# Kernel optimization log

Hardware: AMD Instinct MI355X
Metric: run time of the kernel (lower is better)

## Reference

```python
import jax, jax.numpy as jnp
import numpy as np

S = 4096      # seq_len
D = 1024      # d_model
H = 16        # n_heads
E = 64        # head dim (D // H)
SCALE0 = 1.0 / np.sqrt(E)  # sh_scale_factor


def setup_inputs() -> dict:
    key = jax.random.key(0)
    ks = jax.random.split(key, 10)
    std = 1.0 / np.sqrt(D)
    inputs = jax.random.normal(ks[0], (S, D), dtype=jnp.float32)
    # per-head projection weights stacked over heads: [H, D, E]
    Wq = jax.random.normal(ks[1], (H, D, E), dtype=jnp.float32) * std
    bq = jnp.zeros((H, E), dtype=jnp.float32)
    Wk = jax.random.normal(ks[2], (H, D, E), dtype=jnp.float32) * std
    bk = jnp.zeros((H, E), dtype=jnp.float32)
    Wv = jax.random.normal(ks[3], (H, D, E), dtype=jnp.float32) * std
    bv = jnp.zeros((H, E), dtype=jnp.float32)
    # learned per-head scalar scale, initialized to 1/sqrt(E)
    scale = jnp.full((H,), SCALE0, dtype=jnp.float32)
    # output projection (stored as [D_in, D_out])
    Wo = jax.random.normal(ks[4], (H * E, D), dtype=jnp.float32) * std
    bo = jnp.zeros((D,), dtype=jnp.float32)
    return {"inputs": inputs, "Wq": Wq, "bq": bq, "Wk": Wk, "bk": bk,
            "Wv": Wv, "bv": bv, "scale": scale, "Wo": Wo, "bo": bo}


def reference(inputs, Wq, bq, Wk, bk, Wv, bv, scale, Wo, bo):
    # per-head QKV projections, batched over heads: [H, S, E]
    q = jnp.einsum('sd,hde->hse', inputs, Wq) + bq[:, None, :]
    k = jnp.einsum('sd,hde->hse', inputs, Wk) + bk[:, None, :]
    v = jnp.einsum('sd,hde->hse', inputs, Wv) + bv[:, None, :]
    # scores [H, S, S], learned scalar scale per head, softmax over keys
    scores = jnp.einsum('hqe,hke->hqk', q, k) * scale[:, None, None]
    attn = jax.nn.softmax(scores, axis=-1)
    o = jnp.einsum('hqk,hke->hqe', attn, v)           # [H, S, E]
    o = jnp.transpose(o, (1, 0, 2)).reshape(S, H * E)  # concat heads on dim 1
    return o @ Wo + bo                                 # [S, D]
```

## Files before the change

kernel.cpp:

```cpp
#include <hip/hip_runtime.h>
#include <stdint.h>

#define S_LEN 4096
#define D_MOD 1024
#define NH    16
#define EH    64

typedef short bf16x8 __attribute__((ext_vector_type(8)));
typedef float f32x4  __attribute__((ext_vector_type(4)));
typedef float f32x16 __attribute__((ext_vector_type(16)));

__device__ __forceinline__ unsigned short f2b(float x){
    uint32_t u = __float_as_uint(x);
    u = (u + 0x7fffu + ((u >> 16) & 1u)) >> 16;
    return (unsigned short)u;
}

__device__ __forceinline__ uint32_t cvtpk_bf16(float lo, float hi){
    uint32_t r;
    asm volatile("v_cvt_pk_bf16_f32 %0, %1, %2" : "=v"(r) : "v"(lo), "v"(hi));
    return r;
}

__device__ __forceinline__ void gld_lds16(const void* g, void* l){
    __builtin_amdgcn_global_load_lds((const __attribute__((address_space(1))) void*)g,
                                     (__attribute__((address_space(3))) void*)l, 16, 0, 0);
}

#define PSWAP_U(a, b) asm volatile("v_permlane32_swap_b32 %0, %1" : "+v"(a), "+v"(b))

#define WAITV4() asm volatile("s_waitcnt vmcnt(4)" ::: "memory")
#define WAITV0() asm volatile("s_waitcnt vmcnt(0)" ::: "memory")
#define CFENCE() asm volatile("" ::: "memory")


__global__ void k_conv_all(const float* __restrict__ x, unsigned short* __restrict__ xb,
                           const float* __restrict__ Wq, const float* __restrict__ Wk,
                           const float* __restrict__ Wv, unsigned short* __restrict__ wt,
                           const float* __restrict__ Wo, unsigned short* __restrict__ wot){
    __shared__ float lt[64][65];
    const int tid = threadIdx.x;
    int b = blockIdx.x;
    if (b < 4096){
        int i = (b * 256 + tid) * 4;
        float4 v = *(const float4*)(x + i);
        ushort4 o;
        o.x = f2b(v.x); o.y = f2b(v.y); o.z = f2b(v.z); o.w = f2b(v.w);
        *(ushort4*)(xb + i) = o;
        return;
    }
    b -= 4096;
    if (b < 768){
        const int d0 = (b & 15) * 64;
        const int th = b >> 4;
        const int t = th >> 4, h = th & 15;
        const float* W = (t == 0) ? Wq : ((t == 1) ? Wk : Wv);
        #pragma unroll
        for (int i = 0; i < 16; i++){
            int idx = tid + 256 * i;
            int dl = idx >> 6, e = idx & 63;
            lt[dl][e] = W[((size_t)((h << 10) + d0 + dl) << 6) + e];
        }
        __syncthreads();
        #pragma unroll
        for (int i = 0; i < 16; i++){
            int idx = tid + 256 * i;
            int eo = idx >> 6, dlo = idx & 63;
            wt[((size_t)((t << 10) + (h << 6) + eo) << 10) + d0 + dlo] = f2b(lt[dlo][eo]);
        }
    } else {
        b -= 768;
        const int he0 = (b & 15) * 64, d0 = (b >> 4) * 64;
        #pragma unroll
        for (int i = 0; i < 16; i++){
            int idx = tid + 256 * i;
            int r = idx >> 6, c = idx & 63;
            lt[r][c] = Wo[((size_t)(he0 + r) << 10) + d0 + c];
        }
        __syncthreads();
        #pragma unroll
        for (int i = 0; i < 16; i++){
            int idx = tid + 256 * i;
            int rr = idx >> 6, cc = idx & 63;
            wot[((size_t)(d0 + rr) << 10) + he0 + cc] = f2b(lt[cc][rr]);
        }
    }
}

__global__ void k_tv(const unsigned short* __restrict__ vr, unsigned short* __restrict__ vt){
    __shared__ unsigned short lt[64][66];
    const int tid = threadIdx.x;
    const int s0 = blockIdx.x * 64, h = blockIdx.y;
    #pragma unroll
    for (int i = 0; i < 4; i++){
        int idx = tid + 256 * i;
        int r = idx >> 4, c4 = idx & 15;
        ushort4 v = *(const ushort4*)(vr + (((size_t)(h << 12) + s0 + r) << 6) + c4 * 4);
        lt[r][c4 * 4 + 0] = v.x; lt[r][c4 * 4 + 1] = v.y;
        lt[r][c4 * 4 + 2] = v.z; lt[r][c4 * 4 + 3] = v.w;
    }
    __syncthreads();
    #pragma unroll
    for (int i = 0; i < 4; i++){
        int idx = tid + 256 * i;
        int e = idx >> 4, j4 = idx & 15;
        ushort4 o;
        o.x = lt[j4 * 4 + 0][e]; o.y = lt[j4 * 4 + 1][e];
        o.z = lt[j4 * 4 + 2][e]; o.w = lt[j4 * 4 + 3][e];
        *(ushort4*)(vt + (size_t)((h << 6) + e) * 4096 + s0 + j4 * 4) = o;
    }
}


template<int MODE, int NI>
__global__ __launch_bounds__(256, 4)
void k_gemm(const unsigned short* __restrict__ A, const unsigned short* __restrict__ B, int K,
            unsigned short* __restrict__ qb, unsigned short* __restrict__ kb,
            unsigned short* __restrict__ vr,
            const float* __restrict__ b0, const float* __restrict__ b1, const float* __restrict__ b2,
            const float* __restrict__ scl,
            float* __restrict__ outp, const float* __restrict__ bo){
    __shared__ uint4 lsA4[1024];
    __shared__ uint4 lsB4[NI * 256];
    char* lsA = (char*)lsA4;
    char* lsB = (char*)lsB4;
    const int tid = threadIdx.x;
    const int lane = tid & 63, w = tid >> 6;
    const int lr = lane & 15, lg = lane >> 4;
    const int wm = w >> 1, wn = w & 1;
    const int m0 = blockIdx.y * 128, n0 = blockIdx.x * (32 * NI);
    const int wbase = tid & ~63;

    f32x4 acc[4][NI] = {};

    for (int k0 = 0; k0 < K; k0 += 64){
        __syncthreads();
        #pragma unroll
        for (int i = 0; i < 4; i++){
            int s = tid + 256 * i;
            int row = s >> 3, c = s & 7;
            int cs = c ^ (row & 7);
            gld_lds16(A + (size_t)(m0 + row) * K + k0 + cs * 8, lsA + (wbase + 256 * i) * 16);
        }
        #pragma unroll
        for (int i = 0; i < NI; i++){
            int s = tid + 256 * i;
            int row = s >> 3, c = s & 7;
            int cs = c ^ (row & 7);
            gld_lds16(B + (size_t)(n0 + row) * K + k0 + cs * 8, lsB + (wbase + 256 * i) * 16);
        }
        __syncthreads();
        #pragma unroll
        for (int kc = 0; kc < 2; kc++){
            bf16x8 af[4], bf[NI];
            #pragma unroll
            for (int mi = 0; mi < 4; mi++){
                int row = wm * 64 + mi * 16 + lr;
                int j = kc * 4 + lg;
                af[mi] = *(const bf16x8*)(lsA + row * 128 + (j ^ (row & 7)) * 16);
            }
            #pragma unroll
            for (int ni = 0; ni < NI; ni++){
                int row = wn * (NI * 16) + ni * 16 + lr;
                int j = kc * 4 + lg;
                bf[ni] = *(const bf16x8*)(lsB + row * 128 + (j ^ (row & 7)) * 16);
            }
            #pragma unroll
            for (int mi = 0; mi < 4; mi++)
                #pragma unroll
                for (int ni = 0; ni < NI; ni++)
                    acc[mi][ni] = __builtin_amdgcn_mfma_f32_16x16x32_bf16(af[mi], bf[ni], acc[mi][ni], 0, 0, 0);
        }
    }

    #pragma unroll
    for (int mi = 0; mi < 4; mi++){
        #pragma unroll
        for (int ni = 0; ni < NI; ni++){
            int gnb = n0 + wn * (NI * 16) + ni * 16;
            if (MODE == 0){
                int t = gnb >> 10, h = (gnb >> 6) & 15;
                int e = (gnb & 63) + lr;
                const float* bp = (t == 0) ? b0 : ((t == 1) ? b1 : b2);
                float badd = bp[(h << 6) + e];
                float qs = (t == 0) ? scl[h] * 1.4426950408889634f : 1.0f;
                unsigned short* tgt = (t == 0) ? qb : ((t == 1) ? kb : vr);
                #pragma unroll
                for (int r = 0; r < 4; r++){
                    int gm = m0 + wm * 64 + mi * 16 + lg * 4 + r;
                    tgt[((size_t)((h << 12) + gm) << 6) + e] = f2b((acc[mi][ni][r] + badd) * qs);
                }
            } else {
                int gn = gnb + lr;
                float badd = bo[gn];
                #pragma unroll
                for (int r = 0; r < 4; r++){
                    int gm = m0 + wm * 64 + mi * 16 + lg * 4 + r;
                    outp[(size_t)gm * 1024 + gn] = acc[mi][ni][r] + badd;
                }
            }
        }
    }
}


__global__ __launch_bounds__(256, 4)
void k_attn(const unsigned short* __restrict__ qb, const unsigned short* __restrict__ kb,
            const unsigned short* __restrict__ vt,
            unsigned short* __restrict__ po0, unsigned short* __restrict__ po1,
            float* __restrict__ pl){
    __shared__ uint4 ldsb[2048];
    char* ldsc = (char*)ldsb;

    const int tid = threadIdx.x;
    const int lane = tid & 63, w = tid >> 6;
    const int ql = lane & 31, hi = lane >> 5;

    int wg = blockIdx.y * 64 + blockIdx.x;
    wg = (wg & 7) * 128 + (wg >> 3);
    const int h = wg >> 6;
    const int qblk = (wg & 63) >> 1;
    const int sk = wg & 1;
    const int q0 = qblk * 128 + w * 32;
    const int kbase = sk * 2048;

    bf16x8 qf[4];
    #pragma unroll
    for (int kc = 0; kc < 4; kc++)
        qf[kc] = *(const bf16x8*)(qb + (size_t)((h << 12) + q0 + ql) * 64 + kc * 16 + hi * 8);

    bf16x8 ones;
    #pragma unroll
    for (int j = 0; j < 8; j++) ones[j] = (short)0x3F80;

    f32x16 oacc[2] = {}, lacc = {};

    auto stage = [&](int buf, int kt){
        char* Kd = ldsc + buf * 16384;
        char* Vd = Kd + 8192;
        #pragma unroll
        for (int c = 0; c < 2; c++){
            int g = w * 2 + c;
            const unsigned short* ksrc = kb + ((size_t)(h << 12) + kt + (g >> 2) * 32 + ql) * 64
                                            + (g & 3) * 16 + hi * 8;
            gld_lds16(ksrc, Kd + g * 1024);
            const unsigned short* vsrc = vt + (size_t)((h << 6) + (g >> 2) * 32 + ql) * 4096
                                            + kt + (g & 3) * 16 + hi * 8;
            gld_lds16(vsrc, Vd + g * 1024);
        }
    };

    auto pack2 = [&](f32x16& v, bf16x8& pA, bf16x8& pB){
        #pragma unroll
        for (int r = 0; r < 16; r++)
            v[r] = __builtin_amdgcn_exp2f(v[r]);
        uint32_t a0 = cvtpk_bf16(v[0], v[1]);
        uint32_t a1 = cvtpk_bf16(v[2], v[3]);
        uint32_t b0 = cvtpk_bf16(v[4], v[5]);
        uint32_t b1 = cvtpk_bf16(v[6], v[7]);
        PSWAP_U(a0, b0);
        PSWAP_U(a1, b1);
        uint32_t f0[4] = {a0, a1, b0, b1};
        pA = *(bf16x8*)f0;
        uint32_t c0 = cvtpk_bf16(v[8],  v[9]);
        uint32_t c1 = cvtpk_bf16(v[10], v[11]);
        uint32_t d0 = cvtpk_bf16(v[12], v[13]);
        uint32_t d1 = cvtpk_bf16(v[14], v[15]);
        PSWAP_U(c0, d0);
        PSWAP_U(c1, d1);
        uint32_t f1[4] = {c0, c1, d0, d1};
        pB = *(bf16x8*)f1;
    };

    stage(0, kbase);
    stage(1, kbase + 64);

    int buf = 0;
    for (int t = 0; t < 32; t++){
        if (t < 31) WAITV4();
        else        WAITV0();
        __builtin_amdgcn_s_barrier();
        CFENCE();

        const char* Kc = ldsc + buf * 16384;
        const char* Vc = Kc + 8192;

        f32x16 s0 = {}, s1 = {};
        __builtin_amdgcn_s_setprio(1);
        #pragma unroll
        for (int kc = 0; kc < 4; kc++){
            bf16x8 kf = *(const bf16x8*)(Kc + kc * 1024 + lane * 16);
            s0 = __builtin_amdgcn_mfma_f32_32x32x16_bf16(kf, qf[kc], s0, 0, 0, 0);
        }
        #pragma unroll
        for (int kc = 0; kc < 4; kc++){
            bf16x8 kf = *(const bf16x8*)(Kc + (4 + kc) * 1024 + lane * 16);
            s1 = __builtin_amdgcn_mfma_f32_32x32x16_bf16(kf, qf[kc], s1, 0, 0, 0);
        }
        bf16x8 p00, p01;
        pack2(s0, p00, p01);

        {
            bf16x8 vf0 = *(const bf16x8*)(Vc + (0 * 4 + 0) * 1024 + lane * 16);
            oacc[0] = __builtin_amdgcn_mfma_f32_32x32x16_bf16(vf0, p00, oacc[0], 0, 0, 0);
            bf16x8 vf1 = *(const bf16x8*)(Vc + (1 * 4 + 0) * 1024 + lane * 16);
            oacc[1] = __builtin_amdgcn_mfma_f32_32x32x16_bf16(vf1, p00, oacc[1], 0, 0, 0);
            lacc = __builtin_amdgcn_mfma_f32_32x32x16_bf16(ones, p00, lacc, 0, 0, 0);
            bf16x8 vf2 = *(const bf16x8*)(Vc + (0 * 4 + 1) * 1024 + lane * 16);
            oacc[0] = __builtin_amdgcn_mfma_f32_32x32x16_bf16(vf2, p01, oacc[0], 0, 0, 0);
            bf16x8 vf3 = *(const bf16x8*)(Vc + (1 * 4 + 1) * 1024 + lane * 16);
            oacc[1] = __builtin_amdgcn_mfma_f32_32x32x16_bf16(vf3, p01, oacc[1], 0, 0, 0);
            lacc = __builtin_amdgcn_mfma_f32_32x32x16_bf16(ones, p01, lacc, 0, 0, 0);
        }
        bf16x8 p10, p11;
        pack2(s1, p10, p11);

        {
            bf16x8 vf0 = *(const bf16x8*)(Vc + (0 * 4 + 2) * 1024 + lane * 16);
            oacc[0] = __builtin_amdgcn_mfma_f32_32x32x16_bf16(vf0, p10, oacc[0], 0, 0, 0);
            bf16x8 vf1 = *(const bf16x8*)(Vc + (1 * 4 + 2) * 1024 + lane * 16);
            oacc[1] = __builtin_amdgcn_mfma_f32_32x32x16_bf16(vf1, p10, oacc[1], 0, 0, 0);
            lacc = __builtin_amdgcn_mfma_f32_32x32x16_bf16(ones, p10, lacc, 0, 0, 0);
            bf16x8 vf2 = *(const bf16x8*)(Vc + (0 * 4 + 3) * 1024 + lane * 16);
            oacc[0] = __builtin_amdgcn_mfma_f32_32x32x16_bf16(vf2, p11, oacc[0], 0, 0, 0);
            bf16x8 vf3 = *(const bf16x8*)(Vc + (1 * 4 + 3) * 1024 + lane * 16);
            oacc[1] = __builtin_amdgcn_mfma_f32_32x32x16_bf16(vf3, p11, oacc[1], 0, 0, 0);
            lacc = __builtin_amdgcn_mfma_f32_32x32x16_bf16(ones, p11, lacc, 0, 0, 0);
        }
        __builtin_amdgcn_s_setprio(0);
        CFENCE();

        if (t + 2 < 32){
            __builtin_amdgcn_s_barrier();
            CFENCE();
            stage(buf, kbase + (t + 2) * 64);
        }
        buf ^= 1;
    }

    unsigned short* pout = sk ? po1 : po0;
    if (lane < 32)
        pl[((sk << 4) + h) * 4096 + q0 + ql] = lacc[0];
    #pragma unroll
    for (int et = 0; et < 2; et++){
        #pragma unroll
        for (int g = 0; g < 4; g++){
            ushort4 o4;
            o4.x = f2b(oacc[et][4 * g + 0]);
            o4.y = f2b(oacc[et][4 * g + 1]);
            o4.z = f2b(oacc[et][4 * g + 2]);
            o4.w = f2b(oacc[et][4 * g + 3]);
            int e = et * 32 + 8 * g + 4 * hi;
            *(ushort4*)(pout + (size_t)(q0 + ql) * 1024 + (h << 6) + e) = o4;
        }
    }
}

__global__ void k_comb(const unsigned short* __restrict__ po0, const unsigned short* __restrict__ po1,
                       const float* __restrict__ pl, unsigned short* __restrict__ ob){
    int i = blockIdx.x * 256 + threadIdx.x;
    int s = i >> 7, g8 = i & 127;
    int h = g8 >> 3;
    float inv = 1.0f / (pl[(h << 12) + s] + pl[((16 + h) << 12) + s]);
    size_t off = ((size_t)s << 10) + g8 * 8;
    const ushort4* a = (const ushort4*)(po0 + off);
    const ushort4* b = (const ushort4*)(po1 + off);
    ushort4 o[2];
    #pragma unroll
    for (int k = 0; k < 2; k++){
        ushort4 av = a[k], bv = b[k];
        o[k].x = f2b((__uint_as_float((uint32_t)av.x << 16) + __uint_as_float((uint32_t)bv.x << 16)) * inv);
        o[k].y = f2b((__uint_as_float((uint32_t)av.y << 16) + __uint_as_float((uint32_t)bv.y << 16)) * inv);
        o[k].z = f2b((__uint_as_float((uint32_t)av.z << 16) + __uint_as_float((uint32_t)bv.z << 16)) * inv);
        o[k].w = f2b((__uint_as_float((uint32_t)av.w << 16) + __uint_as_float((uint32_t)bv.w << 16)) * inv);
    }
    *(ushort4*)(ob + off) = o[0];
    *(ushort4*)(ob + off + 4) = o[1];
}


extern "C" void kernel_launch(void* const* d_in, const int* in_sizes, int n_in,
                              void* d_out, int out_size, void* d_ws, size_t ws_size,
                              hipStream_t stream){
    const float* x  = (const float*)d_in[0];
    const float* Wq = (const float*)d_in[1];
    const float* bq = (const float*)d_in[2];
    const float* Wk = (const float*)d_in[3];
    const float* bk = (const float*)d_in[4];
    const float* Wv = (const float*)d_in[5];
    const float* bv = (const float*)d_in[6];
    const float* sc = (const float*)d_in[7];
    const float* Wo = (const float*)d_in[8];
    const float* bo = (const float*)d_in[9];
    float* out = (float*)d_out;
    char* ws = (char*)d_ws;
    const size_t MB = 1u << 20;

    unsigned short* xb  = (unsigned short*)(ws + 0);
    unsigned short* ob  = xb;
    unsigned short* wt  = (unsigned short*)(ws + 8  * MB);
    unsigned short* wot = (unsigned short*)(ws + 14 * MB);
    unsigned short* qb  = (unsigned short*)(ws + 16 * MB);
    unsigned short* kb  = (unsigned short*)(ws + 24 * MB);
    unsigned short* vr  = (unsigned short*)(ws + 32 * MB);
    unsigned short* po0 = vr;
    unsigned short* vt  = (unsigned short*)(ws + 40 * MB);
    unsigned short* po1 = (unsigned short*)(ws + 48 * MB);
    float*          pl  = (float*)(ws + 56 * MB);

    k_conv_all<<<5120, 256, 0, stream>>>(x, xb, Wq, Wk, Wv, wt, Wo, wot);

    k_gemm<0, 4><<<dim3(24, 32), 256, 0, stream>>>(xb, wt, D_MOD, qb, kb, vr, bq, bk, bv, sc, nullptr, nullptr);
    k_tv        <<<dim3(64, 16), 256, 0, stream>>>(vr, vt);
    k_attn      <<<dim3(64, 16), 256, 0, stream>>>(qb, kb, vt, po0, po1, pl);
    k_comb      <<<2048, 256, 0, stream>>>(po0, po1, pl, ob);
    k_gemm<1, 2><<<dim3(16, 32), 256, 0, stream>>>(ob, wot, D_MOD, nullptr, nullptr, nullptr,
                                                   nullptr, nullptr, nullptr, nullptr, out, bo);
}
```

Before: 160.0 us.

## Process two query tiles per wave and replace ones-MFMA row sums with VALU sums

```diff
diff --git a/kernel.cpp b/kernel.cpp
--- a/kernel.cpp
+++ b/kernel.cpp
@@ -28,6 +28,17 @@
 }
 
 #define PSWAP_U(a, b) asm volatile("v_permlane32_swap_b32 %0, %1" : "+v"(a), "+v"(b))
+
+__device__ __forceinline__ float vcopy(float x){
+    float y;
+    asm volatile("v_mov_b32 %0, %1" : "=v"(y) : "v"(x));
+    return y;
+}
+__device__ __forceinline__ float pswap_add(float x){
+    uint32_t a = __float_as_uint(x), b = __float_as_uint(vcopy(x));
+    PSWAP_U(a, b);
+    return __uint_as_float(a) + __uint_as_float(b);
+}
 
 #define WAITV4() asm volatile("s_waitcnt vmcnt(4)" ::: "memory")
 #define WAITV0() asm volatile("s_waitcnt vmcnt(0)" ::: "memory")
@@ -204,7 +215,7 @@
 }
 
 
-__global__ __launch_bounds__(256, 4)
+__global__ __launch_bounds__(256, 2)
 void k_attn(const unsigned short* __restrict__ qb, const unsigned short* __restrict__ kb,
             const unsigned short* __restrict__ vt,
             unsigned short* __restrict__ po0, unsigned short* __restrict__ po1,
@@ -216,24 +227,23 @@
     const int lane = tid & 63, w = tid >> 6;
     const int ql = lane & 31, hi = lane >> 5;
 
-    int wg = blockIdx.y * 64 + blockIdx.x;
-    wg = (wg & 7) * 128 + (wg >> 3);
-    const int h = wg >> 6;
-    const int qblk = (wg & 63) >> 1;
-    const int sk = wg & 1;
-    const int q0 = qblk * 128 + w * 32;
+    int wg = blockIdx.y * 32 + blockIdx.x;
+    wg = (wg & 7) * 64 + (wg >> 3);
+    const int h = wg >> 5;
+    const int rem = wg & 31;
+    const int qblk = rem >> 1, sk = rem & 1;
+    const int q0 = qblk * 256 + w * 64;
     const int kbase = sk * 2048;
 
-    bf16x8 qf[4];
-    #pragma unroll
-    for (int kc = 0; kc < 4; kc++)
-        qf[kc] = *(const bf16x8*)(qb + (size_t)((h << 12) + q0 + ql) * 64 + kc * 16 + hi * 8);
-
-    bf16x8 ones;
-    #pragma unroll
-    for (int j = 0; j < 8; j++) ones[j] = (short)0x3F80;
-
-    f32x16 oacc[2] = {}, lacc = {};
+    bf16x8 qf0[4], qf1[4];
+    #pragma unroll
+    for (int kc = 0; kc < 4; kc++){
+        qf0[kc] = *(const bf16x8*)(qb + (size_t)((h << 12) + q0 + ql) * 64 + kc * 16 + hi * 8);
+        qf1[kc] = *(const bf16x8*)(qb + (size_t)((h << 12) + q0 + 32 + ql) * 64 + kc * 16 + hi * 8);
+    }
+
+    f32x16 o00 = {}, o01 = {}, o10 = {}, o11 = {};
+    float ps0 = 0.f, ps1 = 0.f;
 
     auto stage = [&](int buf, int kt){
         char* Kd = ldsc + buf * 16384;
@@ -250,10 +260,12 @@
         }
     };
 
-    auto pack2 = [&](f32x16& v, bf16x8& pA, bf16x8& pB){
-        #pragma unroll
-        for (int r = 0; r < 16; r++)
+    auto pack2 = [&](f32x16& v, bf16x8& pA, bf16x8& pB, float& psum){
+        #pragma unroll
+        for (int r = 0; r < 16; r++){
             v[r] = __builtin_amdgcn_exp2f(v[r]);
+            psum += v[r];
+        }
         uint32_t a0 = cvtpk_bf16(v[0], v[1]);
         uint32_t a1 = cvtpk_bf16(v[2], v[3]);
         uint32_t b0 = cvtpk_bf16(v[4], v[5]);
@@ -285,47 +297,58 @@
         const char* Kc = ldsc + buf * 16384;
         const char* Vc = Kc + 8192;
 
-        f32x16 s0 = {}, s1 = {};
         __builtin_amdgcn_s_setprio(1);
+        f32x16 s00 = {}, s10 = {};
         #pragma unroll
         for (int kc = 0; kc < 4; kc++){
             bf16x8 kf = *(const bf16x8*)(Kc + kc * 1024 + lane * 16);
-            s0 = __builtin_amdgcn_mfma_f32_32x32x16_bf16(kf, qf[kc], s0, 0, 0, 0);
-        }
+            s00 = __builtin_amdgcn_mfma_f32_32x32x16_bf16(kf, qf0[kc], s00, 0, 0, 0);
+            s10 = __builtin_amdgcn_mfma_f32_32x32x16_bf16(kf, qf1[kc], s10, 0, 0, 0);
+        }
+        f32x16 s01 = {}, s11 = {};
         #pragma unroll
         for (int kc = 0; kc < 4; kc++){
             bf16x8 kf = *(const bf16x8*)(Kc + (4 + kc) * 1024 + lane * 16);
-            s1 = __builtin_amdgcn_mfma_f32_32x32x16_bf16(kf, qf[kc], s1, 0, 0, 0);
-        }
-        bf16x8 p00, p01;
-        pack2(s0, p00, p01);
+            s01 = __builtin_amdgcn_mfma_f32_32x32x16_bf16(kf, qf0[kc], s01, 0, 0, 0);
+            s11 = __builtin_amdgcn_mfma_f32_32x32x16_bf16(kf, qf1[kc], s11, 0, 0, 0);
+        }
+        bf16x8 pA0, pA1, pB0, pB1;
+        pack2(s00, pA0, pA1, ps0);
+        pack2(s10, pB0, pB1, ps1);
 
         {
-            bf16x8 vf0 = *(const bf16x8*)(Vc + (0 * 4 + 0) * 1024 + lane * 16);
-            oacc[0] = __builtin_amdgcn_mfma_f32_32x32x16_bf16(vf0, p00, oacc[0], 0, 0, 0);
-            bf16x8 vf1 = *(const bf16x8*)(Vc + (1 * 4 + 0) * 1024 + lane * 16);
-            oacc[1] = __builtin_amdgcn_mfma_f32_32x32x16_bf16(vf1, p00, oacc[1], 0, 0, 0);
-            lacc = __builtin_amdgcn_mfma_f32_32x32x16_bf16(ones, p00, lacc, 0, 0, 0);
-            bf16x8 vf2 = *(const bf16x8*)(Vc + (0 * 4 + 1) * 1024 + lane * 16);
-            oacc[0] = __builtin_amdgcn_mfma_f32_32x32x16_bf16(vf2, p01, oacc[0], 0, 0, 0);
-            bf16x8 vf3 = *(const bf16x8*)(Vc + (1 * 4 + 1) * 1024 + lane * 16);
-            oacc[1] = __builtin_amdgcn_mfma_f32_32x32x16_bf16(vf3, p01, oacc[1], 0, 0, 0);
-            lacc = __builtin_amdgcn_mfma_f32_32x32x16_bf16(ones, p01, lacc, 0, 0, 0);
-        }
-        bf16x8 p10, p11;
-        pack2(s1, p10, p11);
+            bf16x8 vf;
+            vf = *(const bf16x8*)(Vc + (0 * 4 + 0) * 1024 + lane * 16);
+            o00 = __builtin_amdgcn_mfma_f32_32x32x16_bf16(vf, pA0, o00, 0, 0, 0);
+            o10 = __builtin_amdgcn_mfma_f32_32x32x16_bf16(vf, pB0, o10, 0, 0, 0);
+            vf = *(const bf16x8*)(Vc + (1 * 4 + 0) * 1024 + lane * 16);
+            o01 = __builtin_amdgcn_mfma_f32_32x32x16_bf16(vf, pA0, o01, 0, 0, 0);
+            o11 = __builtin_amdgcn_mfma_f32_32x32x16_bf16(vf, pB0, o11, 0, 0, 0);
+            vf = *(const bf16x8*)(Vc + (0 * 4 + 1) * 1024 + lane * 16);
+            o00 = __builtin_amdgcn_mfma_f32_32x32x16_bf16(vf, pA1, o00, 0, 0, 0);
+            o10 = __builtin_amdgcn_mfma_f32_32x32x16_bf16(vf, pB1, o10, 0, 0, 0);
+            vf = *(const bf16x8*)(Vc + (1 * 4 + 1) * 1024 + lane * 16);
+            o01 = __builtin_amdgcn_mfma_f32_32x32x16_bf16(vf, pA1, o01, 0, 0, 0);
+            o11 = __builtin_amdgcn_mfma_f32_32x32x16_bf16(vf, pB1, o11, 0, 0, 0);
+        }
+        bf16x8 pA2, pA3, pB2, pB3;
+        pack2(s01, pA2, pA3, ps0);
+        pack2(s11, pB2, pB3, ps1);
 
         {
-            bf16x8 vf0 = *(const bf16x8*)(Vc + (0 * 4 + 2) * 1024 + lane * 16);
-            oacc[0] = __builtin_amdgcn_mfma_f32_32x32x16_bf16(vf0, p10, oacc[0], 0, 0, 0);
-            bf16x8 vf1 = *(const bf16x8*)(Vc + (1 * 4 + 2) * 1024 + lane * 16);
-            oacc[1] = __builtin_amdgcn_mfma_f32_32x32x16_bf16(vf1, p10, oacc[1], 0, 0, 0);
-            lacc = __builtin_amdgcn_mfma_f32_32x32x16_bf16(ones, p10, lacc, 0, 0, 0);
-            bf16x8 vf2 = *(const bf16x8*)(Vc + (0 * 4 + 3) * 1024 + lane * 16);
-            oacc[0] = __builtin_amdgcn_mfma_f32_32x32x16_bf16(vf2, p11, oacc[0], 0, 0, 0);
-            bf16x8 vf3 = *(const bf16x8*)(Vc + (1 * 4 + 3) * 1024 + lane * 16);
-            oacc[1] = __builtin_amdgcn_mfma_f32_32x32x16_bf16(vf3, p11, oacc[1], 0, 0, 0);
-            lacc = __builtin_amdgcn_mfma_f32_32x32x16_bf16(ones, p11, lacc, 0, 0, 0);
+            bf16x8 vf;
+            vf = *(const bf16x8*)(Vc + (0 * 4 + 2) * 1024 + lane * 16);
+            o00 = __builtin_amdgcn_mfma_f32_32x32x16_bf16(vf, pA2, o00, 0, 0, 0);
+            o10 = __builtin_amdgcn_mfma_f32_32x32x16_bf16(vf, pB2, o10, 0, 0, 0);
+            vf = *(const bf16x8*)(Vc + (1 * 4 + 2) * 1024 + lane * 16);
+            o01 = __builtin_amdgcn_mfma_f32_32x32x16_bf16(vf, pA2, o01, 0, 0, 0);
+            o11 = __builtin_amdgcn_mfma_f32_32x32x16_bf16(vf, pB2, o11, 0, 0, 0);
+            vf = *(const bf16x8*)(Vc + (0 * 4 + 3) * 1024 + lane * 16);
+            o00 = __builtin_amdgcn_mfma_f32_32x32x16_bf16(vf, pA3, o00, 0, 0, 0);
+            o10 = __builtin_amdgcn_mfma_f32_32x32x16_bf16(vf, pB3, o10, 0, 0, 0);
+            vf = *(const bf16x8*)(Vc + (1 * 4 + 3) * 1024 + lane * 16);
+            o01 = __builtin_amdgcn_mfma_f32_32x32x16_bf16(vf, pA3, o01, 0, 0, 0);
+            o11 = __builtin_amdgcn_mfma_f32_32x32x16_bf16(vf, pB3, o11, 0, 0, 0);
         }
         __builtin_amdgcn_s_setprio(0);
         CFENCE();
@@ -339,19 +362,28 @@
     }
 
     unsigned short* pout = sk ? po1 : po0;
-    if (lane < 32)
-        pl[((sk << 4) + h) * 4096 + q0 + ql] = lacc[0];
-    #pragma unroll
-    for (int et = 0; et < 2; et++){
-        #pragma unroll
-        for (int g = 0; g < 4; g++){
-            ushort4 o4;
-            o4.x = f2b(oacc[et][4 * g + 0]);
-            o4.y = f2b(oacc[et][4 * g + 1]);
-            o4.z = f2b(oacc[et][4 * g + 2]);
-            o4.w = f2b(oacc[et][4 * g + 3]);
-            int e = et * 32 + 8 * g + 4 * hi;
-            *(ushort4*)(pout + (size_t)(q0 + ql) * 1024 + (h << 6) + e) = o4;
+    float l0 = pswap_add(ps0);
+    float l1 = pswap_add(ps1);
+    if (lane < 32){
+        pl[((sk << 4) + h) * 4096 + q0 + ql]      = l0;
+        pl[((sk << 4) + h) * 4096 + q0 + 32 + ql] = l1;
+    }
+    #pragma unroll
+    for (int hf = 0; hf < 2; hf++){
+        int qrow = q0 + hf * 32 + ql;
+        #pragma unroll
+        for (int et = 0; et < 2; et++){
+            const f32x16& o = hf ? (et ? o11 : o10) : (et ? o01 : o00);
+            #pragma unroll
+            for (int g = 0; g < 4; g++){
+                ushort4 o4;
+                o4.x = f2b(o[4 * g + 0]);
+                o4.y = f2b(o[4 * g + 1]);
+                o4.z = f2b(o[4 * g + 2]);
+                o4.w = f2b(o[4 * g + 3]);
+                int e = et * 32 + 8 * g + 4 * hi;
+                *(ushort4*)(pout + (size_t)qrow * 1024 + (h << 6) + e) = o4;
+            }
         }
     }
 }
@@ -412,7 +444,7 @@
 
     k_gemm<0, 4><<<dim3(24, 32), 256, 0, stream>>>(xb, wt, D_MOD, qb, kb, vr, bq, bk, bv, sc, nullptr, nullptr);
     k_tv        <<<dim3(64, 16), 256, 0, stream>>>(vr, vt);
-    k_attn      <<<dim3(64, 16), 256, 0, stream>>>(qb, kb, vt, po0, po1, pl);
+    k_attn      <<<dim3(32, 16), 256, 0, stream>>>(qb, kb, vt, po0, po1, pl);
     k_comb      <<<2048, 256, 0, stream>>>(po0, po1, pl, ob);
     k_gemm<1, 2><<<dim3(16, 32), 256, 0, stream>>>(ob, wot, D_MOD, nullptr, nullptr, nullptr,
                                                    nullptr, nullptr, nullptr, nullptr, out, bo);
```

Measured after the change: 146.0 us. 1.1x faster.
